# Kernel optimization log

Measured on AMD Instinct MI355X. Metric: run time of the kernel, lower is better.

Reference implementation:

```python
import jax, jax.numpy as jnp
import numpy as np

N_NODES = 100000


def setup_inputs() -> dict:
    key = jax.random.key(0)
    k1, k2, k3, k4, k5 = jax.random.split(key, 5)
    in_dim, out_dim, n_edges = 128, 128, 640000
    x = jax.random.normal(k1, (N_NODES, in_dim), dtype=jnp.float32)
    src = jax.random.randint(k2, (n_edges,), 0, N_NODES, dtype=jnp.int32)
    dst = jax.random.randint(k3, (n_edges,), 0, N_NODES, dtype=jnp.int32)
    edge_index = jnp.stack([src, dst], axis=0)  # [2, E]
    # nn.Linear default init: U(-1/sqrt(in_dim), 1/sqrt(in_dim))
    bound = 1.0 / np.sqrt(in_dim)
    W = jax.random.uniform(k4, (out_dim, in_dim), minval=-bound, maxval=bound, dtype=jnp.float32)
    b = jax.random.uniform(k5, (out_dim,), minval=-bound, maxval=bound, dtype=jnp.float32)
    return {"x": x, "edge_index": edge_index, "W": W, "b": b}


def reference(x, edge_index, W, b):
    src, dst = edge_index[0], edge_index[1]
    # scatter-sum of gathered source features into destination nodes
    agg = jax.ops.segment_sum(x[src], dst, num_segments=N_NODES)       # [N, d]
    deg = jax.ops.segment_sum(jnp.ones((src.shape[0], 1), x.dtype), dst,
                              num_segments=N_NODES)                     # [N, 1]
    deg = jnp.maximum(deg, 1.0)
    h = agg / deg + x                                                   # mean-agg + residual
    out = jax.nn.relu(h @ W.T + b)                                      # linear + relu (dropout p=0)
    return out
```

## Files before the change

### kernel.cpp

```cpp
#include <hip/hip_runtime.h>
#include <hip/hip_bf16.h>

constexpr int N_NODES = 100000;
constexpr int DIM     = 128;
constexpr int N_EDGES = 640000;

constexpr int CHUNK     = 1024;
constexpr int N_CHUNKS  = (N_NODES + CHUNK - 1) / CHUNK;
constexpr int BINCAP    = 8192;
constexpr int EPB       = 1024;
constexpr int SRC_BITS  = 17;
constexpr int SRC_MASK  = (1 << SRC_BITS) - 1;

constexpr int XCONV_XBLOCKS = N_NODES * DIM / (256 * 8);
constexpr int XCONV_WBLOCKS = DIM * DIM / (256 * 8);

typedef __attribute__((ext_vector_type(4))) float        f32x4;
typedef __attribute__((ext_vector_type(8))) short        bf16x8;
typedef __attribute__((ext_vector_type(4))) unsigned int u32x4;

static __device__ inline unsigned short f2bf(float f) {
    __hip_bfloat16 h = __float2bfloat16(f);
    return *reinterpret_cast<unsigned short*>(&h);
}
static __device__ inline float bf_lo(unsigned u) { return __uint_as_float(u << 16); }
static __device__ inline float bf_hi(unsigned u) { return __uint_as_float(u & 0xffff0000u); }

__global__ __launch_bounds__(256) void gcn_conv(const float* __restrict__ x,
                                                const float* __restrict__ W,
                                                unsigned int* __restrict__ xb,
                                                unsigned int* __restrict__ wb,
                                                int* __restrict__ bincur)
{
    const int b   = blockIdx.x;
    const int gid = b * 256 + threadIdx.x;

    if (b == 0 && threadIdx.x < 128) bincur[threadIdx.x] = 0;

    const float*  src;
    unsigned int* dst;
    int i;
    if (b < XCONV_XBLOCKS) {
        src = x;  dst = xb;  i = gid;
    } else {
        src = W;  dst = wb;  i = gid - XCONV_XBLOCKS * 256;
    }
    const f32x4* s4 = reinterpret_cast<const f32x4*>(src);
    f32x4 a = s4[2 * i];
    f32x4 c = s4[2 * i + 1];
    u32x4 o;
    o.x = (unsigned)f2bf(a.x) | ((unsigned)f2bf(a.y) << 16);
    o.y = (unsigned)f2bf(a.z) | ((unsigned)f2bf(a.w) << 16);
    o.z = (unsigned)f2bf(c.x) | ((unsigned)f2bf(c.y) << 16);
    o.w = (unsigned)f2bf(c.z) | ((unsigned)f2bf(c.w) << 16);
    reinterpret_cast<u32x4*>(dst)[i] = o;
}

__global__ __launch_bounds__(256) void gcn_bin(const int* __restrict__ src,
                                               const int* __restrict__ dst,
                                               int* __restrict__ bincur,
                                               unsigned int* __restrict__ bindata)
{
    __shared__ int bh[N_CHUNKS];
    __shared__ int btb[N_CHUNKS];

    const int t  = threadIdx.x;
    const int e0 = blockIdx.x * EPB + t * 4;

    if (t < N_CHUNKS) bh[t] = 0;
    __syncthreads();

    const int4 s4 = *reinterpret_cast<const int4*>(src + e0);
    const int4 d4 = *reinterpret_cast<const int4*>(dst + e0);

    int bin[4], pos[4];
    unsigned pv[4];
    const int ds[4] = {d4.x, d4.y, d4.z, d4.w};
    const int ss[4] = {s4.x, s4.y, s4.z, s4.w};
    #pragma unroll
    for (int q = 0; q < 4; ++q) {
        bin[q] = ds[q] >> 10;
        pv[q]  = (unsigned)ss[q] | ((unsigned)(ds[q] & (CHUNK - 1)) << SRC_BITS);
        pos[q] = atomicAdd(&bh[bin[q]], 1);
    }
    __syncthreads();

    if (t < N_CHUNKS) btb[t] = atomicAdd(&bincur[t], bh[t]);
    __syncthreads();

    #pragma unroll
    for (int q = 0; q < 4; ++q)
        bindata[(size_t)bin[q] * BINCAP + btb[bin[q]] + pos[q]] = pv[q];
}

__global__ __launch_bounds__(256) void gcn_build(const int* __restrict__ bincur,
                                                 unsigned int* __restrict__ bindata,
                                                 int* __restrict__ off)
{
    __shared__ unsigned stage[BINCAP];
    __shared__ int hist[CHUNK];
    __shared__ int s[256];

    const int c  = blockIdx.x;
    const int t  = threadIdx.x;
    const int nb = min(bincur[c], BINCAP);
    unsigned int* region = bindata + (size_t)c * BINCAP;

    for (int e = t; e < nb; e += 256) stage[e] = region[e];
    #pragma unroll
    for (int q = 0; q < 4; ++q) hist[t + 256 * q] = 0;
    __syncthreads();

    for (int e = t; e < nb; e += 256)
        atomicAdd(&hist[stage[e] >> SRC_BITS], 1);
    __syncthreads();

    int h0 = hist[4 * t + 0], h1 = hist[4 * t + 1];
    int h2 = hist[4 * t + 2], h3 = hist[4 * t + 3];
    s[t] = h0 + h1 + h2 + h3;
    __syncthreads();
    for (int d = 1; d < 256; d <<= 1) {
        int add = (t >= d) ? s[t - d] : 0;
        __syncthreads();
        s[t] += add;
        __syncthreads();
    }
    int excl = (t > 0) ? s[t - 1] : 0;

    const int st0 = excl;
    const int st1 = excl + h0;
    const int st2 = excl + h0 + h1;
    const int st3 = excl + h0 + h1 + h2;
    hist[4 * t + 0] = st0;  hist[4 * t + 1] = st1;
    hist[4 * t + 2] = st2;  hist[4 * t + 3] = st3;

    const int nbase = c * CHUNK;
    if (nbase + 4 * t + 0 < N_NODES) off[nbase + 4 * t + 0] = st0 | (h0 << 13);
    if (nbase + 4 * t + 1 < N_NODES) off[nbase + 4 * t + 1] = st1 | (h1 << 13);
    if (nbase + 4 * t + 2 < N_NODES) off[nbase + 4 * t + 2] = st2 | (h2 << 13);
    if (nbase + 4 * t + 3 < N_NODES) off[nbase + 4 * t + 3] = st3 | (h3 << 13);
    __syncthreads();

    for (int e = t; e < nb; e += 256) {
        unsigned v  = stage[e];
        int slot    = atomicAdd(&hist[v >> SRC_BITS], 1);
        region[slot] = v & SRC_MASK;
    }
}

static __device__ inline void acc8(float* acc, u32x4 v) {
    #pragma unroll
    for (int q = 0; q < 4; ++q) {
        unsigned u = v[q];
        acc[2 * q]     += bf_lo(u);
        acc[2 * q + 1] += bf_hi(u);
    }
}

__global__ __launch_bounds__(256) void gcn_gather(
    const unsigned short* __restrict__ xb,
    const int* __restrict__ off,
    const unsigned int* __restrict__ csr,
    unsigned int* __restrict__ hb)
{
    const int tid  = threadIdx.x;
    const int lane = tid & 15;
    const int n    = blockIdx.x * 16 + (tid >> 4);

    const int meta  = off[n];
    const int count = meta >> 13;
    const int start = (n >> 10) * BINCAP + (meta & (BINCAP - 1));
    const int end   = start + count;
    const int col8  = lane * 8;

    float acc[8];
    #pragma unroll
    for (int q = 0; q < 8; ++q) acc[q] = 0.0f;

    int i = start;
    for (; i + 4 <= end; i += 4) {
        int s0 = csr[i], s1 = csr[i + 1], s2 = csr[i + 2], s3 = csr[i + 3];
        u32x4 v0 = *reinterpret_cast<const u32x4*>(xb + (size_t)s0 * DIM + col8);
        u32x4 v1 = *reinterpret_cast<const u32x4*>(xb + (size_t)s1 * DIM + col8);
        u32x4 v2 = *reinterpret_cast<const u32x4*>(xb + (size_t)s2 * DIM + col8);
        u32x4 v3 = *reinterpret_cast<const u32x4*>(xb + (size_t)s3 * DIM + col8);
        acc8(acc, v0); acc8(acc, v1); acc8(acc, v2); acc8(acc, v3);
    }
    for (; i < end; ++i) {
        int s = csr[i];
        u32x4 v = *reinterpret_cast<const u32x4*>(xb + (size_t)s * DIM + col8);
        acc8(acc, v);
    }

    const float inv = 1.0f / fmaxf((float)count, 1.0f);
    const u32x4 xr = *reinterpret_cast<const u32x4*>(xb + (size_t)n * DIM + col8);

    u32x4 o;
    #pragma unroll
    for (int q = 0; q < 4; ++q) {
        float h0 = acc[2 * q]     * inv + bf_lo(xr[q]);
        float h1 = acc[2 * q + 1] * inv + bf_hi(xr[q]);
        o[q] = (unsigned)f2bf(h0) | ((unsigned)f2bf(h1) << 16);
    }
    reinterpret_cast<u32x4*>(hb)[(size_t)n * (DIM / 8) + lane] = o;
}

constexpr int N_TILES = N_NODES / 16;

__global__ __launch_bounds__(256) void gcn_mfma(
    const short* __restrict__ hb,
    const short* __restrict__ wb,
    const float* __restrict__ bias,
    float* __restrict__ out)
{
    const int wid  = threadIdx.x >> 6;
    const int lane = threadIdx.x & 63;
    const int tile = blockIdx.x * 4 + wid;
    if (tile >= N_TILES) return;
    const int row0 = tile * 16;

    const int r = lane & 15;
    const int g = lane >> 4;

    bf16x8 wf[8][4];
    #pragma unroll
    for (int c = 0; c < 8; ++c)
        #pragma unroll
        for (int t = 0; t < 4; ++t)
            wf[c][t] = *reinterpret_cast<const bf16x8*>(
                wb + (16 * c + r) * DIM + 32 * t + 8 * g);

    bf16x8 af[4];
    #pragma unroll
    for (int t = 0; t < 4; ++t)
        af[t] = *reinterpret_cast<const bf16x8*>(
            hb + (size_t)(row0 + r) * DIM + 32 * t + 8 * g);

    f32x4 acc[8];
    #pragma unroll
    for (int c = 0; c < 8; ++c) acc[c] = {0.f, 0.f, 0.f, 0.f};

    #pragma unroll
    for (int t = 0; t < 4; ++t)
        #pragma unroll
        for (int c = 0; c < 8; ++c)
            acc[c] = __builtin_amdgcn_mfma_f32_16x16x32_bf16(af[t], wf[c][t], acc[c], 0, 0, 0);

    #pragma unroll
    for (int c = 0; c < 8; ++c) {
        const float bj = bias[16 * c + r];
        #pragma unroll
        for (int q = 0; q < 4; ++q)
            out[(size_t)(row0 + 4 * g + q) * DIM + 16 * c + r] =
                fmaxf(acc[c][q] + bj, 0.0f);
    }
}

extern "C" void kernel_launch(void* const* d_in, const int* in_sizes, int n_in,
                              void* d_out, int out_size, void* d_ws, size_t ws_size,
                              hipStream_t stream)
{
    const float* x    = (const float*)d_in[0];
    const int*   eidx = (const int*)d_in[1];
    const float* W    = (const float*)d_in[2];
    const float* bias = (const float*)d_in[3];
    float*       out  = (float*)d_out;

    const int* src = eidx;
    const int* dst = eidx + N_EDGES;

    int* bincur = (int*)d_ws;
    int* off    = bincur + 128;
    unsigned int* bindata = (unsigned int*)(off + 100352);
    unsigned short* wb = (unsigned short*)(bindata + (size_t)N_CHUNKS * BINCAP);
    unsigned short* hb = wb + (size_t)DIM * DIM;

    unsigned short* xb = (unsigned short*)d_out;

    gcn_conv <<<XCONV_XBLOCKS + XCONV_WBLOCKS, 256, 0, stream>>>(
        x, W, (unsigned int*)xb, (unsigned int*)wb, bincur);
    gcn_bin  <<<N_EDGES / EPB, 256, 0, stream>>>(src, dst, bincur, bindata);
    gcn_build<<<N_CHUNKS, 256, 0, stream>>>(bincur, bindata, off);
    gcn_gather<<<N_NODES / 16, 256, 0, stream>>>(xb, off, bindata, (unsigned int*)hb);
    gcn_mfma <<<(N_TILES + 3) / 4, 256, 0, stream>>>(
        (const short*)hb, (const short*)wb, bias, out);
}
```

Before: 108.3 us.

## Fuse neighbor gather and MFMA linear into one kernel via LDS staging

The gather/mean/residual kernel and the bf16 MFMA linear kernel are merged. Each block of 64 nodes builds its aggregated rows in padded shared memory, then its four waves run the 16x128x128 MFMA tile from LDS. This removes the global write and read of the intermediate h buffer and one launch. It also moves the bf16 copy of x from the output buffer into workspace, since the fused kernel writes out while it still reads x. In exchange, W fragments are now loaded inside the MFMA loop rather than preloaded, and a block barrier separates the latency-bound gather phase from the compute phase.

```diff
diff --git a/kernel.cpp b/kernel.cpp
--- a/kernel.cpp
+++ b/kernel.cpp
@@ -14,6 +14,10 @@
 
 constexpr int XCONV_XBLOCKS = N_NODES * DIM / (256 * 8);
 constexpr int XCONV_WBLOCKS = DIM * DIM / (256 * 8);
+
+constexpr int FUSE_NODES  = 64;
+constexpr int FUSE_BLOCKS = (N_NODES + FUSE_NODES - 1) / FUSE_NODES;
+constexpr int HPAD        = DIM + 8;
 
 typedef __attribute__((ext_vector_type(4))) float        f32x4;
 typedef __attribute__((ext_vector_type(8))) short        bf16x8;
@@ -157,102 +161,98 @@
     }
 }
 
-__global__ __launch_bounds__(256) void gcn_gather(
+__global__ __launch_bounds__(256) void gcn_gmm(
     const unsigned short* __restrict__ xb,
     const int* __restrict__ off,
     const unsigned int* __restrict__ csr,
-    unsigned int* __restrict__ hb)
-{
-    const int tid  = threadIdx.x;
-    const int lane = tid & 15;
-    const int n    = blockIdx.x * 16 + (tid >> 4);
-
-    const int meta  = off[n];
-    const int count = meta >> 13;
-    const int start = (n >> 10) * BINCAP + (meta & (BINCAP - 1));
-    const int end   = start + count;
-    const int col8  = lane * 8;
-
-    float acc[8];
-    #pragma unroll
-    for (int q = 0; q < 8; ++q) acc[q] = 0.0f;
-
-    int i = start;
-    for (; i + 4 <= end; i += 4) {
-        int s0 = csr[i], s1 = csr[i + 1], s2 = csr[i + 2], s3 = csr[i + 3];
-        u32x4 v0 = *reinterpret_cast<const u32x4*>(xb + (size_t)s0 * DIM + col8);
-        u32x4 v1 = *reinterpret_cast<const u32x4*>(xb + (size_t)s1 * DIM + col8);
-        u32x4 v2 = *reinterpret_cast<const u32x4*>(xb + (size_t)s2 * DIM + col8);
-        u32x4 v3 = *reinterpret_cast<const u32x4*>(xb + (size_t)s3 * DIM + col8);
-        acc8(acc, v0); acc8(acc, v1); acc8(acc, v2); acc8(acc, v3);
-    }
-    for (; i < end; ++i) {
-        int s = csr[i];
-        u32x4 v = *reinterpret_cast<const u32x4*>(xb + (size_t)s * DIM + col8);
-        acc8(acc, v);
-    }
-
-    const float inv = 1.0f / fmaxf((float)count, 1.0f);
-    const u32x4 xr = *reinterpret_cast<const u32x4*>(xb + (size_t)n * DIM + col8);
-
-    u32x4 o;
-    #pragma unroll
-    for (int q = 0; q < 4; ++q) {
-        float h0 = acc[2 * q]     * inv + bf_lo(xr[q]);
-        float h1 = acc[2 * q + 1] * inv + bf_hi(xr[q]);
-        o[q] = (unsigned)f2bf(h0) | ((unsigned)f2bf(h1) << 16);
-    }
-    reinterpret_cast<u32x4*>(hb)[(size_t)n * (DIM / 8) + lane] = o;
-}
-
-constexpr int N_TILES = N_NODES / 16;
-
-__global__ __launch_bounds__(256) void gcn_mfma(
-    const short* __restrict__ hb,
-    const short* __restrict__ wb,
+    const unsigned short* __restrict__ wb,
     const float* __restrict__ bias,
     float* __restrict__ out)
 {
-    const int wid  = threadIdx.x >> 6;
-    const int lane = threadIdx.x & 63;
-    const int tile = blockIdx.x * 4 + wid;
-    if (tile >= N_TILES) return;
-    const int row0 = tile * 16;
-
-    const int r = lane & 15;
-    const int g = lane >> 4;
-
-    bf16x8 wf[8][4];
-    #pragma unroll
-    for (int c = 0; c < 8; ++c)
+    __shared__ unsigned short hl[FUSE_NODES][HPAD];
+
+    const int tid  = threadIdx.x;
+    const int n0   = blockIdx.x * FUSE_NODES;
+    const int lane16 = tid & 15;
+    const int col8   = lane16 * 8;
+
+    #pragma unroll
+    for (int sweep = 0; sweep < 4; ++sweep) {
+        const int nloc = sweep * 16 + (tid >> 4);
+        const int n    = n0 + nloc;
+        if (n < N_NODES) {
+            const int meta  = off[n];
+            const int count = meta >> 13;
+            const int start = (n >> 10) * BINCAP + (meta & (BINCAP - 1));
+            const int end   = start + count;
+
+            float acc[8];
+            #pragma unroll
+            for (int q = 0; q < 8; ++q) acc[q] = 0.0f;
+
+            int i = start;
+            for (; i + 4 <= end; i += 4) {
+                int s0 = csr[i], s1 = csr[i + 1], s2 = csr[i + 2], s3 = csr[i + 3];
+                u32x4 v0 = *reinterpret_cast<const u32x4*>(xb + (size_t)s0 * DIM + col8);
+                u32x4 v1 = *reinterpret_cast<const u32x4*>(xb + (size_t)s1 * DIM + col8);
+                u32x4 v2 = *reinterpret_cast<const u32x4*>(xb + (size_t)s2 * DIM + col8);
+                u32x4 v3 = *reinterpret_cast<const u32x4*>(xb + (size_t)s3 * DIM + col8);
+                acc8(acc, v0); acc8(acc, v1); acc8(acc, v2); acc8(acc, v3);
+            }
+            for (; i < end; ++i) {
+                u32x4 v = *reinterpret_cast<const u32x4*>(xb + (size_t)csr[i] * DIM + col8);
+                acc8(acc, v);
+            }
+
+            const float inv = 1.0f / fmaxf((float)count, 1.0f);
+            const u32x4 xr = *reinterpret_cast<const u32x4*>(xb + (size_t)n * DIM + col8);
+            u32x4 o;
+            #pragma unroll
+            for (int q = 0; q < 4; ++q) {
+                float v0 = acc[2 * q]     * inv + bf_lo(xr[q]);
+                float v1 = acc[2 * q + 1] * inv + bf_hi(xr[q]);
+                o[q] = (unsigned)f2bf(v0) | ((unsigned)f2bf(v1) << 16);
+            }
+            *reinterpret_cast<u32x4*>(&hl[nloc][col8]) = o;
+        }
+    }
+    __syncthreads();
+
+    const int w    = tid >> 6;
+    const int lane = tid & 63;
+    const int r    = lane & 15;
+    const int g    = lane >> 4;
+    const int rowbase = n0 + 16 * w;
+    if (rowbase >= N_NODES) return;
+
+    bf16x8 af[4];
+    #pragma unroll
+    for (int t = 0; t < 4; ++t)
+        af[t] = *reinterpret_cast<const bf16x8*>(&hl[16 * w + r][32 * t + 8 * g]);
+
+    f32x4 acc[8];
+    #pragma unroll
+    for (int c = 0; c < 8; ++c) acc[c] = {0.f, 0.f, 0.f, 0.f};
+
+    #pragma unroll
+    for (int c = 0; c < 8; ++c) {
         #pragma unroll
-        for (int t = 0; t < 4; ++t)
-            wf[c][t] = *reinterpret_cast<const bf16x8*>(
+        for (int t = 0; t < 4; ++t) {
+            bf16x8 wf = *reinterpret_cast<const bf16x8*>(
                 wb + (16 * c + r) * DIM + 32 * t + 8 * g);
-
-    bf16x8 af[4];
-    #pragma unroll
-    for (int t = 0; t < 4; ++t)
-        af[t] = *reinterpret_cast<const bf16x8*>(
-            hb + (size_t)(row0 + r) * DIM + 32 * t + 8 * g);
-
-    f32x4 acc[8];
-    #pragma unroll
-    for (int c = 0; c < 8; ++c) acc[c] = {0.f, 0.f, 0.f, 0.f};
-
-    #pragma unroll
-    for (int t = 0; t < 4; ++t)
-        #pragma unroll
-        for (int c = 0; c < 8; ++c)
-            acc[c] = __builtin_amdgcn_mfma_f32_16x16x32_bf16(af[t], wf[c][t], acc[c], 0, 0, 0);
+            acc[c] = __builtin_amdgcn_mfma_f32_16x16x32_bf16(af[t], wf, acc[c], 0, 0, 0);
+        }
+    }
 
     #pragma unroll
     for (int c = 0; c < 8; ++c) {
         const float bj = bias[16 * c + r];
         #pragma unroll
-        for (int q = 0; q < 4; ++q)
-            out[(size_t)(row0 + 4 * g + q) * DIM + 16 * c + r] =
-                fmaxf(acc[c][q] + bj, 0.0f);
+        for (int q = 0; q < 4; ++q) {
+            const int n = rowbase + 4 * g + q;
+            if (n < N_NODES)
+                out[(size_t)n * DIM + 16 * c + r] = fmaxf(acc[c][q] + bj, 0.0f);
+        }
     }
 }
 
@@ -273,15 +273,12 @@
     int* off    = bincur + 128;
     unsigned int* bindata = (unsigned int*)(off + 100352);
     unsigned short* wb = (unsigned short*)(bindata + (size_t)N_CHUNKS * BINCAP);
-    unsigned short* hb = wb + (size_t)DIM * DIM;
-
-    unsigned short* xb = (unsigned short*)d_out;
+    unsigned short* xb = wb + (size_t)DIM * DIM;
 
     gcn_conv <<<XCONV_XBLOCKS + XCONV_WBLOCKS, 256, 0, stream>>>(
         x, W, (unsigned int*)xb, (unsigned int*)wb, bincur);
     gcn_bin  <<<N_EDGES / EPB, 256, 0, stream>>>(src, dst, bincur, bindata);
     gcn_build<<<N_CHUNKS, 256, 0, stream>>>(bincur, bindata, off);
-    gcn_gather<<<N_NODES / 16, 256, 0, stream>>>(xb, off, bindata, (unsigned int*)hb);
-    gcn_mfma <<<(N_TILES + 3) / 4, 256, 0, stream>>>(
-        (const short*)hb, (const short*)wb, bias, out);
-}
+    gcn_gmm  <<<FUSE_BLOCKS, 256, 0, stream>>>(
+        xb, off, bindata, wb, bias, out);
+}
```

Result: slower. 119.0 us (+9.9%).
